# Kernel optimization log

Hardware: AMD Instinct MI355X
Metric: run time of the kernel (lower is better)

Reference implementation:

```python
import jax, jax.numpy as jnp
import numpy as np
import math

EMB = 256
H = 2
DH = EMB // H  # 128; seq_len must equal DH due to matmul(q,k) without transpose
B = 1024
S = DH


def setup_inputs() -> dict:
    key = jax.random.key(0)
    ks = jax.random.split(key, 12)
    sc = 1.0 / math.sqrt(EMB)
    return {
        "q": jax.random.normal(ks[0], (B, S, EMB), jnp.float32),
        "k": jax.random.normal(ks[1], (B, S, EMB), jnp.float32),
        "v": jax.random.normal(ks[2], (B, S, EMB), jnp.float32),
        "attention_mask": jax.random.randint(ks[3], (B, S), 0, 2, jnp.int32),
        "Wq": jax.random.normal(ks[4], (EMB, EMB), jnp.float32) * sc,
        "bq": jnp.zeros((EMB,), jnp.float32),
        "Wk": jax.random.normal(ks[5], (EMB, EMB), jnp.float32) * sc,
        "bk": jnp.zeros((EMB,), jnp.float32),
        "Wv": jax.random.normal(ks[6], (EMB, EMB), jnp.float32) * sc,
        "bv": jnp.zeros((EMB,), jnp.float32),
        "Wo": jax.random.normal(ks[7], (EMB, EMB), jnp.float32) * sc,
        "bo": jnp.zeros((EMB,), jnp.float32),
    }


def reference(q, k, v, attention_mask, Wq, bq, Wk, bk, Wv, bv, Wo, bo):
    b, s, _ = q.shape
    qp = (q @ Wq + bq) * (1.0 / math.sqrt(EMB))  # scale by sqrt(all_head_size)
    kp = k @ Wk + bk
    vp = v @ Wv + bv  # projected but unused downstream (faithful to source)
    # [B,S,E] -> [B,H,S,DH]
    qh = qp.reshape(b, s, H, DH).transpose(0, 2, 1, 3)
    kh = kp.reshape(b, s, H, DH).transpose(0, 2, 1, 3)
    # matmul WITHOUT transposing k: contract q's head dim with k's seq dim
    scores = jnp.einsum("bhsm,bhmj->bhsj", qh, kh)  # [B,H,S,DH]
    # additive mask: +1.0 where attention_mask == 0 (quirk of source)
    mask_add = (attention_mask == 0).astype(jnp.float32)[:, None, None, :]
    probs = jax.nn.softmax(scores + mask_add, axis=-1)  # [B,H,S,DH]
    out = probs.transpose(0, 2, 1, 3).reshape(b, s, H * DH)
    return out @ Wo + bo
```

## Files before the change

### kernel.cpp

```cpp
#include <hip/hip_runtime.h>
#include <hip/hip_bf16.h>

#define NB 1024
#define NS 128
#define NE 256

typedef __attribute__((ext_vector_type(8))) short bf16x8;
typedef __attribute__((ext_vector_type(4))) float f32x4;

__device__ __forceinline__ unsigned short f2bf(float x) {
  unsigned int u = __float_as_uint(x);
  u = (u + 0x7fffu + ((u >> 16) & 1u)) >> 16;
  return (unsigned short)u;
}

__global__ void prep_weights(const float* __restrict__ Wq,
                             const float* __restrict__ Wk,
                             const float* __restrict__ Wo,
                             short* __restrict__ WqT,
                             short* __restrict__ WkT,
                             short* __restrict__ WoT) {
  int idx = blockIdx.x * blockDim.x + threadIdx.x;
  int n = idx >> 8;
  int kk = idx & 255;
  WqT[idx] = (short)f2bf(Wq[kk * NE + n]);
  WkT[idx] = (short)f2bf(Wk[kk * NE + n]);
  WoT[idx] = (short)f2bf(Wo[kk * NE + n]);
}

__device__ __forceinline__ void stage_tile(const float* __restrict__ src,
                                           char* __restrict__ dst, int t) {
  #pragma unroll
  for (int i = 0; i < 16; ++i) {
    int idx = t + i * 512;
    float4 v = reinterpret_cast<const float4*>(src)[idx];
    int row = idx >> 6;
    int colb = (idx & 63) << 3;
    ushort4 u;
    u.x = f2bf(v.x); u.y = f2bf(v.y); u.z = f2bf(v.z); u.w = f2bf(v.w);
    *reinterpret_cast<ushort4*>(dst + row * 512 + (colb ^ ((row & 7) << 4))) = u;
  }
}

__device__ __forceinline__ void gemm_8x16(const char* __restrict__ ldsA,
                                          const short* __restrict__ BT,
                                          int wr, int wc, int cl, int c4,
                                          f32x4 acc[4][4]) {
  #pragma unroll
  for (int ks = 0; ks < 8; ++ks) {
    const int kel = ks * 32 + 8 * c4;
    bf16x8 a[4], bb[4];
    #pragma unroll
    for (int mi = 0; mi < 4; ++mi) {
      int row = wr * 64 + mi * 16 + cl;
      a[mi] = *reinterpret_cast<const bf16x8*>(
          ldsA + row * 512 + ((kel * 2) ^ ((row & 7) << 4)));
    }
    #pragma unroll
    for (int ni = 0; ni < 4; ++ni) {
      int col = wc * 64 + ni * 16 + cl;
      bb[ni] = *reinterpret_cast<const bf16x8*>(BT + col * 256 + kel);
    }
    #pragma unroll
    for (int mi = 0; mi < 4; ++mi)
      #pragma unroll
      for (int ni = 0; ni < 4; ++ni)
        acc[mi][ni] = __builtin_amdgcn_mfma_f32_16x16x32_bf16(
            a[mi], bb[ni], acc[mi][ni], 0, 0, 0);
  }
}

__global__ __launch_bounds__(512, 2)
void fused_attn(const float* __restrict__ q,
                const float* __restrict__ kin,
                const int* __restrict__ am,
                const float* __restrict__ bq,
                const float* __restrict__ bk,
                const float* __restrict__ bo,
                const short* __restrict__ WqT,
                const short* __restrict__ WkT,
                const short* __restrict__ WoT,
                float* __restrict__ out) {
  extern __shared__ char lds[];
  char* stA = lds;
  char* kpT = lds + 65536;

  const int t = threadIdx.x;
  const int lane = t & 63;
  const int wid = t >> 6;
  const int cl = lane & 15;
  const int c4 = lane >> 4;
  const int wr = wid >> 2;
  const int wc = wid & 3;
  const int b = blockIdx.x;

  f32x4 acc[4][4];

  stage_tile(kin + (size_t)b * (NS * NE), stA, t);
  __syncthreads();

  #pragma unroll
  for (int mi = 0; mi < 4; ++mi)
    #pragma unroll
    for (int ni = 0; ni < 4; ++ni) acc[mi][ni] = (f32x4){0.f, 0.f, 0.f, 0.f};
  gemm_8x16(stA, WkT, wr, wc, cl, c4, acc);
  #pragma unroll
  for (int mi = 0; mi < 4; ++mi)
    #pragma unroll
    for (int ni = 0; ni < 4; ++ni) {
      int ce = wc * 64 + ni * 16 + cl;
      float bkv = bk[ce];
      int h = ce >> 7, j = ce & 127;
      char* base = kpT + h * 32768 + j * 256;
      int sw = (j & 7) << 4;
      #pragma unroll
      for (int r = 0; r < 4; ++r) {
        int seq = wr * 64 + mi * 16 + c4 * 4 + r;
        *reinterpret_cast<unsigned short*>(base + ((seq * 2) ^ sw)) =
            f2bf(acc[mi][ni][r] + bkv);
      }
    }
  __syncthreads();

  stage_tile(q + (size_t)b * (NS * NE), stA, t);
  __syncthreads();

  #pragma unroll
  for (int mi = 0; mi < 4; ++mi)
    #pragma unroll
    for (int ni = 0; ni < 4; ++ni) acc[mi][ni] = (f32x4){0.f, 0.f, 0.f, 0.f};
  gemm_8x16(stA, WqT, wr, wc, cl, c4, acc);
  __syncthreads();
  #pragma unroll
  for (int mi = 0; mi < 4; ++mi)
    #pragma unroll
    for (int ni = 0; ni < 4; ++ni) {
      int ce = wc * 64 + ni * 16 + cl;
      float bqv = bq[ce];
      int ceb = ce * 2;
      #pragma unroll
      for (int r = 0; r < 4; ++r) {
        int seq = wr * 64 + mi * 16 + c4 * 4 + r;
        *reinterpret_cast<unsigned short*>(
            stA + seq * 512 + (ceb ^ ((seq & 7) << 4))) =
            f2bf((acc[mi][ni][r] + bqv) * 0.0625f);
      }
    }
  __syncthreads();

  {
    f32x4 sacc[2][8];
    #pragma unroll
    for (int h = 0; h < 2; ++h)
      #pragma unroll
      for (int ni = 0; ni < 8; ++ni) sacc[h][ni] = (f32x4){0.f, 0.f, 0.f, 0.f};
    const int arow = wid * 16 + cl;
    #pragma unroll
    for (int h = 0; h < 2; ++h) {
      #pragma unroll
      for (int ks = 0; ks < 4; ++ks) {
        int kel = h * 128 + ks * 32 + 8 * c4;
        bf16x8 a = *reinterpret_cast<const bf16x8*>(
            stA + arow * 512 + ((kel * 2) ^ ((arow & 7) << 4)));
        int kb = (ks * 32 + 8 * c4) * 2;
        #pragma unroll
        for (int ni = 0; ni < 8; ++ni) {
          int jr = ni * 16 + cl;
          bf16x8 bbv = *reinterpret_cast<const bf16x8*>(
              kpT + h * 32768 + jr * 256 + (kb ^ ((jr & 7) << 4)));
          sacc[h][ni] = __builtin_amdgcn_mfma_f32_16x16x32_bf16(
              a, bbv, sacc[h][ni], 0, 0, 0);
        }
      }
    }
    float madd[8];
    #pragma unroll
    for (int ni = 0; ni < 8; ++ni)
      madd[ni] = (am[b * NS + ni * 16 + cl] == 0) ? 1.0f : 0.0f;
    #pragma unroll
    for (int h = 0; h < 2; ++h) {
      #pragma unroll
      for (int r = 0; r < 4; ++r) {
        float m = -1e30f;
        #pragma unroll
        for (int ni = 0; ni < 8; ++ni) m = fmaxf(m, sacc[h][ni][r] + madd[ni]);
        #pragma unroll
        for (int d = 1; d < 16; d <<= 1) m = fmaxf(m, __shfl_xor(m, d, 64));
        float s = 0.f;
        #pragma unroll
        for (int ni = 0; ni < 8; ++ni) {
          float e = __expf(sacc[h][ni][r] + madd[ni] - m);
          sacc[h][ni][r] = e;
          s += e;
        }
        #pragma unroll
        for (int d = 1; d < 16; d <<= 1) s += __shfl_xor(s, d, 64);
        float rinv = 1.0f / s;
        #pragma unroll
        for (int ni = 0; ni < 8; ++ni) sacc[h][ni][r] *= rinv;
      }
    }
    #pragma unroll
    for (int h = 0; h < 2; ++h)
      #pragma unroll
      for (int ni = 0; ni < 8; ++ni)
        #pragma unroll
        for (int r = 0; r < 4; ++r) {
          int seq = wid * 16 + c4 * 4 + r;
          int ceb = (h * 128 + ni * 16 + cl) * 2;
          *reinterpret_cast<unsigned short*>(
              stA + seq * 512 + (ceb ^ ((seq & 7) << 4))) =
              f2bf(sacc[h][ni][r]);
        }
  }
  __syncthreads();

  #pragma unroll
  for (int mi = 0; mi < 4; ++mi)
    #pragma unroll
    for (int ni = 0; ni < 4; ++ni) acc[mi][ni] = (f32x4){0.f, 0.f, 0.f, 0.f};
  gemm_8x16(stA, WoT, wr, wc, cl, c4, acc);
  float* ob = out + (size_t)b * (NS * NE);
  #pragma unroll
  for (int mi = 0; mi < 4; ++mi)
    #pragma unroll
    for (int ni = 0; ni < 4; ++ni) {
      int ce = wc * 64 + ni * 16 + cl;
      float bov = bo[ce];
      #pragma unroll
      for (int r = 0; r < 4; ++r) {
        int seq = wr * 64 + mi * 16 + c4 * 4 + r;
        ob[seq * NE + ce] = acc[mi][ni][r] + bov;
      }
    }
}

extern "C" void kernel_launch(void* const* d_in, const int* in_sizes, int n_in,
                              void* d_out, int out_size, void* d_ws, size_t ws_size,
                              hipStream_t stream) {
  const float* q  = (const float*)d_in[0];
  const float* k  = (const float*)d_in[1];
  const int*   am = (const int*)d_in[3];
  const float* Wq = (const float*)d_in[4];
  const float* bq = (const float*)d_in[5];
  const float* Wk = (const float*)d_in[6];
  const float* bk = (const float*)d_in[7];
  const float* Wo = (const float*)d_in[10];
  const float* bo = (const float*)d_in[11];
  float* out = (float*)d_out;

  short* WqT = (short*)d_ws;
  short* WkT = WqT + NE * NE;
  short* WoT = WkT + NE * NE;

  prep_weights<<<NE * NE / 256, 256, 0, stream>>>(Wq, Wk, Wo, WqT, WkT, WoT);

  (void)hipFuncSetAttribute((const void*)fused_attn,
                            hipFuncAttributeMaxDynamicSharedMemorySize, 131072);
  fused_attn<<<NB, 512, 131072, stream>>>(q, k, am, bq, bk, bo,
                                          WqT, WkT, WoT, out);
}
```

Baseline: 194.1 us.

## Use 1024-thread blocks, prefetch q into registers during k staging

Doubles the block to 16 waves. Each wave now owns a 32x64 output tile, and in the scores stage each wave handles one head and one 16-row tile. Both the k and q tiles are loaded from global memory at the start, with q held in registers while the K projection runs, so the second global load latency is hidden. K-projection results are written to LDS as packed ushort4 stores. The goal is more waves to hide latency and fewer exposed load phases, at the cost of higher register pressure (launch_bounds 1024 with a min of 4) and 128KB of LDS per block, which limits residency to one block per CU.

```diff
diff --git a/kernel.cpp b/kernel.cpp
--- a/kernel.cpp
+++ b/kernel.cpp
@@ -28,31 +28,17 @@
   WoT[idx] = (short)f2bf(Wo[kk * NE + n]);
 }
 
-__device__ __forceinline__ void stage_tile(const float* __restrict__ src,
-                                           char* __restrict__ dst, int t) {
-  #pragma unroll
-  for (int i = 0; i < 16; ++i) {
-    int idx = t + i * 512;
-    float4 v = reinterpret_cast<const float4*>(src)[idx];
-    int row = idx >> 6;
-    int colb = (idx & 63) << 3;
-    ushort4 u;
-    u.x = f2bf(v.x); u.y = f2bf(v.y); u.z = f2bf(v.z); u.w = f2bf(v.w);
-    *reinterpret_cast<ushort4*>(dst + row * 512 + (colb ^ ((row & 7) << 4))) = u;
-  }
-}
-
-__device__ __forceinline__ void gemm_8x16(const char* __restrict__ ldsA,
-                                          const short* __restrict__ BT,
-                                          int wr, int wc, int cl, int c4,
-                                          f32x4 acc[4][4]) {
+__device__ __forceinline__ void gemm_2x4(const char* __restrict__ ldsA,
+                                         const short* __restrict__ BT,
+                                         int wr, int wc, int cl, int c4,
+                                         f32x4 acc[2][4]) {
   #pragma unroll
   for (int ks = 0; ks < 8; ++ks) {
     const int kel = ks * 32 + 8 * c4;
-    bf16x8 a[4], bb[4];
-    #pragma unroll
-    for (int mi = 0; mi < 4; ++mi) {
-      int row = wr * 64 + mi * 16 + cl;
+    bf16x8 a[2], bb[4];
+    #pragma unroll
+    for (int mi = 0; mi < 2; ++mi) {
+      int row = wr * 32 + mi * 16 + cl;
       a[mi] = *reinterpret_cast<const bf16x8*>(
           ldsA + row * 512 + ((kel * 2) ^ ((row & 7) << 4)));
     }
@@ -62,7 +48,7 @@
       bb[ni] = *reinterpret_cast<const bf16x8*>(BT + col * 256 + kel);
     }
     #pragma unroll
-    for (int mi = 0; mi < 4; ++mi)
+    for (int mi = 0; mi < 2; ++mi)
       #pragma unroll
       for (int ni = 0; ni < 4; ++ni)
         acc[mi][ni] = __builtin_amdgcn_mfma_f32_16x16x32_bf16(
@@ -70,7 +56,7 @@
   }
 }
 
-__global__ __launch_bounds__(512, 2)
+__global__ __launch_bounds__(1024, 4)
 void fused_attn(const float* __restrict__ q,
                 const float* __restrict__ kin,
                 const int* __restrict__ am,
@@ -82,8 +68,8 @@
                 const short* __restrict__ WoT,
                 float* __restrict__ out) {
   extern __shared__ char lds[];
-  char* stA = lds;
-  char* kpT = lds + 65536;
+  char* ST = lds;
+  char* KT = lds + 65536;
 
   const int t = threadIdx.x;
   const int lane = t & 63;
@@ -94,45 +80,72 @@
   const int wc = wid & 3;
   const int b = blockIdx.x;
 
-  f32x4 acc[4][4];
-
-  stage_tile(kin + (size_t)b * (NS * NE), stA, t);
-  __syncthreads();
-
-  #pragma unroll
-  for (int mi = 0; mi < 4; ++mi)
+  const float* qb = q + (size_t)b * (NS * NE);
+  const float* kb = kin + (size_t)b * (NS * NE);
+
+  f32x4 acc[2][4];
+
+  float4 qv[8];
+  {
+    const float4* k4 = reinterpret_cast<const float4*>(kb);
+    const float4* q4 = reinterpret_cast<const float4*>(qb);
+    #pragma unroll
+    for (int i = 0; i < 8; ++i) {
+      int idx = t + i * 1024;
+      float4 v = k4[idx];
+      qv[i] = q4[idx];
+      int row = idx >> 6;
+      int colb = (idx & 63) << 3;
+      ushort4 u;
+      u.x = f2bf(v.x); u.y = f2bf(v.y); u.z = f2bf(v.z); u.w = f2bf(v.w);
+      *reinterpret_cast<ushort4*>(ST + row * 512 + (colb ^ ((row & 7) << 4))) = u;
+    }
+  }
+  __syncthreads();
+
+  #pragma unroll
+  for (int mi = 0; mi < 2; ++mi)
     #pragma unroll
     for (int ni = 0; ni < 4; ++ni) acc[mi][ni] = (f32x4){0.f, 0.f, 0.f, 0.f};
-  gemm_8x16(stA, WkT, wr, wc, cl, c4, acc);
-  #pragma unroll
-  for (int mi = 0; mi < 4; ++mi)
+  gemm_2x4(ST, WkT, wr, wc, cl, c4, acc);
+  #pragma unroll
+  for (int mi = 0; mi < 2; ++mi)
     #pragma unroll
     for (int ni = 0; ni < 4; ++ni) {
       int ce = wc * 64 + ni * 16 + cl;
       float bkv = bk[ce];
       int h = ce >> 7, j = ce & 127;
-      char* base = kpT + h * 32768 + j * 256;
-      int sw = (j & 7) << 4;
-      #pragma unroll
-      for (int r = 0; r < 4; ++r) {
-        int seq = wr * 64 + mi * 16 + c4 * 4 + r;
-        *reinterpret_cast<unsigned short*>(base + ((seq * 2) ^ sw)) =
-            f2bf(acc[mi][ni][r] + bkv);
-      }
-    }
-  __syncthreads();
-
-  stage_tile(q + (size_t)b * (NS * NE), stA, t);
-  __syncthreads();
-
-  #pragma unroll
-  for (int mi = 0; mi < 4; ++mi)
+      int seq0 = wr * 32 + mi * 16 + c4 * 4;
+      ushort4 u;
+      u.x = f2bf(acc[mi][ni][0] + bkv);
+      u.y = f2bf(acc[mi][ni][1] + bkv);
+      u.z = f2bf(acc[mi][ni][2] + bkv);
+      u.w = f2bf(acc[mi][ni][3] + bkv);
+      *reinterpret_cast<ushort4*>(
+          KT + h * 32768 + j * 256 + ((seq0 * 2) ^ ((j & 7) << 4))) = u;
+    }
+  __syncthreads();
+
+  #pragma unroll
+  for (int i = 0; i < 8; ++i) {
+    int idx = t + i * 1024;
+    int row = idx >> 6;
+    int colb = (idx & 63) << 3;
+    ushort4 u;
+    u.x = f2bf(qv[i].x); u.y = f2bf(qv[i].y);
+    u.z = f2bf(qv[i].z); u.w = f2bf(qv[i].w);
+    *reinterpret_cast<ushort4*>(ST + row * 512 + (colb ^ ((row & 7) << 4))) = u;
+  }
+  __syncthreads();
+
+  #pragma unroll
+  for (int mi = 0; mi < 2; ++mi)
     #pragma unroll
     for (int ni = 0; ni < 4; ++ni) acc[mi][ni] = (f32x4){0.f, 0.f, 0.f, 0.f};
-  gemm_8x16(stA, WqT, wr, wc, cl, c4, acc);
-  __syncthreads();
-  #pragma unroll
-  for (int mi = 0; mi < 4; ++mi)
+  gemm_2x4(ST, WqT, wr, wc, cl, c4, acc);
+  __syncthreads();
+  #pragma unroll
+  for (int mi = 0; mi < 2; ++mi)
     #pragma unroll
     for (int ni = 0; ni < 4; ++ni) {
       int ce = wc * 64 + ni * 16 + cl;
@@ -140,37 +153,34 @@
       int ceb = ce * 2;
       #pragma unroll
       for (int r = 0; r < 4; ++r) {
-        int seq = wr * 64 + mi * 16 + c4 * 4 + r;
+        int seq = wr * 32 + mi * 16 + c4 * 4 + r;
         *reinterpret_cast<unsigned short*>(
-            stA + seq * 512 + (ceb ^ ((seq & 7) << 4))) =
+            ST + seq * 512 + (ceb ^ ((seq & 7) << 4))) =
             f2bf((acc[mi][ni][r] + bqv) * 0.0625f);
       }
     }
   __syncthreads();
 
   {
-    f32x4 sacc[2][8];
-    #pragma unroll
-    for (int h = 0; h < 2; ++h)
-      #pragma unroll
-      for (int ni = 0; ni < 8; ++ni) sacc[h][ni] = (f32x4){0.f, 0.f, 0.f, 0.f};
-    const int arow = wid * 16 + cl;
-    #pragma unroll
-    for (int h = 0; h < 2; ++h) {
-      #pragma unroll
-      for (int ks = 0; ks < 4; ++ks) {
-        int kel = h * 128 + ks * 32 + 8 * c4;
-        bf16x8 a = *reinterpret_cast<const bf16x8*>(
-            stA + arow * 512 + ((kel * 2) ^ ((arow & 7) << 4)));
-        int kb = (ks * 32 + 8 * c4) * 2;
-        #pragma unroll
-        for (int ni = 0; ni < 8; ++ni) {
-          int jr = ni * 16 + cl;
-          bf16x8 bbv = *reinterpret_cast<const bf16x8*>(
-              kpT + h * 32768 + jr * 256 + (kb ^ ((jr & 7) << 4)));
-          sacc[h][ni] = __builtin_amdgcn_mfma_f32_16x16x32_bf16(
-              a, bbv, sacc[h][ni], 0, 0, 0);
-        }
+    const int h = wid >> 3;
+    const int rt = wid & 7;
+    f32x4 sacc[8];
+    #pragma unroll
+    for (int ni = 0; ni < 8; ++ni) sacc[ni] = (f32x4){0.f, 0.f, 0.f, 0.f};
+    const int arow = rt * 16 + cl;
+    #pragma unroll
+    for (int ks = 0; ks < 4; ++ks) {
+      int kel = h * 128 + ks * 32 + 8 * c4;
+      bf16x8 a = *reinterpret_cast<const bf16x8*>(
+          ST + arow * 512 + ((kel * 2) ^ ((arow & 7) << 4)));
+      int kb2 = (ks * 32 + 8 * c4) * 2;
+      #pragma unroll
+      for (int ni = 0; ni < 8; ++ni) {
+        int jr = ni * 16 + cl;
+        bf16x8 bbv = *reinterpret_cast<const bf16x8*>(
+            KT + h * 32768 + jr * 256 + (kb2 ^ ((jr & 7) << 4)));
+        sacc[ni] = __builtin_amdgcn_mfma_f32_16x16x32_bf16(
+            a, bbv, sacc[ni], 0, 0, 0);
       }
     }
     float madd[8];
@@ -178,58 +188,52 @@
     for (int ni = 0; ni < 8; ++ni)
       madd[ni] = (am[b * NS + ni * 16 + cl] == 0) ? 1.0f : 0.0f;
     #pragma unroll
-    for (int h = 0; h < 2; ++h) {
+    for (int r = 0; r < 4; ++r) {
+      float m = -1e30f;
+      #pragma unroll
+      for (int ni = 0; ni < 8; ++ni) m = fmaxf(m, sacc[ni][r] + madd[ni]);
+      #pragma unroll
+      for (int d = 1; d < 16; d <<= 1) m = fmaxf(m, __shfl_xor(m, d, 64));
+      float s = 0.f;
+      #pragma unroll
+      for (int ni = 0; ni < 8; ++ni) {
+        float e = __expf(sacc[ni][r] + madd[ni] - m);
+        sacc[ni][r] = e;
+        s += e;
+      }
+      #pragma unroll
+      for (int d = 1; d < 16; d <<= 1) s += __shfl_xor(s, d, 64);
+      float rinv = 1.0f / s;
+      #pragma unroll
+      for (int ni = 0; ni < 8; ++ni) sacc[ni][r] *= rinv;
+    }
+    #pragma unroll
+    for (int ni = 0; ni < 8; ++ni)
       #pragma unroll
       for (int r = 0; r < 4; ++r) {
-        float m = -1e30f;
-        #pragma unroll
-        for (int ni = 0; ni < 8; ++ni) m = fmaxf(m, sacc[h][ni][r] + madd[ni]);
-        #pragma unroll
-        for (int d = 1; d < 16; d <<= 1) m = fmaxf(m, __shfl_xor(m, d, 64));
-        float s = 0.f;
-        #pragma unroll
-        for (int ni = 0; ni < 8; ++ni) {
-          float e = __expf(sacc[h][ni][r] + madd[ni] - m);
-          sacc[h][ni][r] = e;
-          s += e;
-        }
-        #pragma unroll
-        for (int d = 1; d < 16; d <<= 1) s += __shfl_xor(s, d, 64);
-        float rinv = 1.0f / s;
-        #pragma unroll
-        for (int ni = 0; ni < 8; ++ni) sacc[h][ni][r] *= rinv;
-      }
-    }
-    #pragma unroll
-    for (int h = 0; h < 2; ++h)
-      #pragma unroll
-      for (int ni = 0; ni < 8; ++ni)
-        #pragma unroll
-        for (int r = 0; r < 4; ++r) {
-          int seq = wid * 16 + c4 * 4 + r;
-          int ceb = (h * 128 + ni * 16 + cl) * 2;
-          *reinterpret_cast<unsigned short*>(
-              stA + seq * 512 + (ceb ^ ((seq & 7) << 4))) =
-              f2bf(sacc[h][ni][r]);
-        }
-  }
-  __syncthreads();
-
-  #pragma unroll
-  for (int mi = 0; mi < 4; ++mi)
+        int row = rt * 16 + c4 * 4 + r;
+        int ceb = (h * 128 + ni * 16 + cl) * 2;
+        *reinterpret_cast<unsigned short*>(
+            ST + row * 512 + (ceb ^ ((row & 7) << 4))) = f2bf(sacc[ni][r]);
+      }
+  }
+  __syncthreads();
+
+  #pragma unroll
+  for (int mi = 0; mi < 2; ++mi)
     #pragma unroll
     for (int ni = 0; ni < 4; ++ni) acc[mi][ni] = (f32x4){0.f, 0.f, 0.f, 0.f};
-  gemm_8x16(stA, WoT, wr, wc, cl, c4, acc);
+  gemm_2x4(ST, WoT, wr, wc, cl, c4, acc);
   float* ob = out + (size_t)b * (NS * NE);
   #pragma unroll
-  for (int mi = 0; mi < 4; ++mi)
+  for (int mi = 0; mi < 2; ++mi)
     #pragma unroll
     for (int ni = 0; ni < 4; ++ni) {
       int ce = wc * 64 + ni * 16 + cl;
       float bov = bo[ce];
       #pragma unroll
       for (int r = 0; r < 4; ++r) {
-        int seq = wr * 64 + mi * 16 + c4 * 4 + r;
+        int seq = wr * 32 + mi * 16 + c4 * 4 + r;
         ob[seq * NE + ce] = acc[mi][ni][r] + bov;
       }
     }
@@ -257,6 +261,6 @@
 
   (void)hipFuncSetAttribute((const void*)fused_attn,
                             hipFuncAttributeMaxDynamicSharedMemorySize, 131072);
-  fused_attn<<<NB, 512, 131072, stream>>>(q, k, am, bq, bk, bo,
-                                          WqT, WkT, WoT, out);
-}
+  fused_attn<<<NB, 1024, 131072, stream>>>(q, k, am, bq, bk, bo,
+                                           WqT, WkT, WoT, out);
+}
```

New measurement: 275.3 us. 1.42x slower.

## Split fused attention into parallel QK projection and attention-output kernels

Applied to the files above, without the earlier changes.

Splits the single fused kernel into two. The first launches two blocks per batch, one projecting K (stored transposed) and one projecting Q, writing bf16 results to workspace. The second reloads them, runs scores, softmax and the output projection. Each kernel now uses 64KB of LDS instead of 128KB, allowing more resident blocks and twice as many blocks in the projection stage. The cost is an extra global round-trip of roughly 128MB of bf16 intermediates. The old fused kernel is kept as a fallback when the workspace is too small.

```diff
diff --git a/kernel.cpp b/kernel.cpp
--- a/kernel.cpp
+++ b/kernel.cpp
@@ -68,6 +68,208 @@
         acc[mi][ni] = __builtin_amdgcn_mfma_f32_16x16x32_bf16(
             a[mi], bb[ni], acc[mi][ni], 0, 0, 0);
   }
+}
+
+__global__ __launch_bounds__(512, 4)
+void proj_qk(const float* __restrict__ q,
+             const float* __restrict__ kin,
+             const float* __restrict__ bq,
+             const float* __restrict__ bk,
+             const short* __restrict__ WqT,
+             const short* __restrict__ WkT,
+             short* __restrict__ QP,
+             short* __restrict__ KPT) {
+  extern __shared__ char ST[];
+  const int t = threadIdx.x;
+  const int lane = t & 63;
+  const int wid = t >> 6;
+  const int cl = lane & 15;
+  const int c4 = lane >> 4;
+  const int b = blockIdx.x >> 1;
+
+  if ((blockIdx.x & 1) == 0) {
+    stage_tile(kin + (size_t)b * (NS * NE), ST, t);
+    __syncthreads();
+    const int we = wid >> 1;
+    const int wm = wid & 1;
+    f32x4 acc[4][4];
+    #pragma unroll
+    for (int ei = 0; ei < 4; ++ei)
+      #pragma unroll
+      for (int mi = 0; mi < 4; ++mi) acc[ei][mi] = (f32x4){0.f, 0.f, 0.f, 0.f};
+    #pragma unroll
+    for (int ks = 0; ks < 8; ++ks) {
+      const int kel = ks * 32 + 8 * c4;
+      bf16x8 a[4], bb[4];
+      #pragma unroll
+      for (int ei = 0; ei < 4; ++ei) {
+        int er = we * 64 + ei * 16 + cl;
+        a[ei] = *reinterpret_cast<const bf16x8*>(WkT + er * 256 + kel);
+      }
+      #pragma unroll
+      for (int mi = 0; mi < 4; ++mi) {
+        int mr = wm * 64 + mi * 16 + cl;
+        bb[mi] = *reinterpret_cast<const bf16x8*>(
+            ST + mr * 512 + ((kel * 2) ^ ((mr & 7) << 4)));
+      }
+      #pragma unroll
+      for (int ei = 0; ei < 4; ++ei)
+        #pragma unroll
+        for (int mi = 0; mi < 4; ++mi)
+          acc[ei][mi] = __builtin_amdgcn_mfma_f32_16x16x32_bf16(
+              a[ei], bb[mi], acc[ei][mi], 0, 0, 0);
+    }
+    short* kp = KPT + (size_t)b * (NE * NS);
+    #pragma unroll
+    for (int ei = 0; ei < 4; ++ei)
+      #pragma unroll
+      for (int r = 0; r < 4; ++r) {
+        int e = we * 64 + ei * 16 + c4 * 4 + r;
+        float bkv = bk[e];
+        #pragma unroll
+        for (int mi = 0; mi < 4; ++mi) {
+          int m = wm * 64 + mi * 16 + cl;
+          kp[e * NS + m] = (short)f2bf(acc[ei][mi][r] + bkv);
+        }
+      }
+  } else {
+    stage_tile(q + (size_t)b * (NS * NE), ST, t);
+    __syncthreads();
+    const int wr = wid >> 2, wc = wid & 3;
+    f32x4 acc[4][4];
+    #pragma unroll
+    for (int mi = 0; mi < 4; ++mi)
+      #pragma unroll
+      for (int ni = 0; ni < 4; ++ni) acc[mi][ni] = (f32x4){0.f, 0.f, 0.f, 0.f};
+    gemm_8x16(ST, WqT, wr, wc, cl, c4, acc);
+    char* qp = (char*)QP + (size_t)b * 65536;
+    #pragma unroll
+    for (int mi = 0; mi < 4; ++mi)
+      #pragma unroll
+      for (int ni = 0; ni < 4; ++ni) {
+        int ce = wc * 64 + ni * 16 + cl;
+        float bqv = bq[ce];
+        #pragma unroll
+        for (int r = 0; r < 4; ++r) {
+          int seq = wr * 64 + mi * 16 + c4 * 4 + r;
+          *reinterpret_cast<unsigned short*>(
+              qp + seq * 512 + ((ce * 2) ^ ((seq & 7) << 4))) =
+              f2bf((acc[mi][ni][r] + bqv) * 0.0625f);
+        }
+      }
+  }
+}
+
+__global__ __launch_bounds__(512, 4)
+void attn_out(const short* __restrict__ QP,
+              const short* __restrict__ KPT,
+              const int* __restrict__ am,
+              const float* __restrict__ bo,
+              const short* __restrict__ WoT,
+              float* __restrict__ out) {
+  extern __shared__ char ST[];
+  const int t = threadIdx.x;
+  const int lane = t & 63;
+  const int wid = t >> 6;
+  const int cl = lane & 15;
+  const int c4 = lane >> 4;
+  const int b = blockIdx.x;
+
+  {
+    const int4* src = reinterpret_cast<const int4*>((const char*)QP + (size_t)b * 65536);
+    int4* dst = reinterpret_cast<int4*>(ST);
+    #pragma unroll
+    for (int i = 0; i < 8; ++i) dst[t + i * 512] = src[t + i * 512];
+  }
+  __syncthreads();
+
+  {
+    const short* kp = KPT + (size_t)b * (NE * NS);
+    f32x4 sacc[2][8];
+    #pragma unroll
+    for (int h = 0; h < 2; ++h)
+      #pragma unroll
+      for (int ni = 0; ni < 8; ++ni) sacc[h][ni] = (f32x4){0.f, 0.f, 0.f, 0.f};
+    const int arow = wid * 16 + cl;
+    #pragma unroll
+    for (int h = 0; h < 2; ++h) {
+      #pragma unroll
+      for (int ks = 0; ks < 4; ++ks) {
+        int kel = h * 128 + ks * 32 + 8 * c4;
+        bf16x8 a = *reinterpret_cast<const bf16x8*>(
+            ST + arow * 512 + ((kel * 2) ^ ((arow & 7) << 4)));
+        int mel = ks * 32 + 8 * c4;
+        #pragma unroll
+        for (int ni = 0; ni < 8; ++ni) {
+          int jr = ni * 16 + cl;
+          bf16x8 bbv = *reinterpret_cast<const bf16x8*>(
+              kp + (h * 128 + jr) * NS + mel);
+          sacc[h][ni] = __builtin_amdgcn_mfma_f32_16x16x32_bf16(
+              a, bbv, sacc[h][ni], 0, 0, 0);
+        }
+      }
+    }
+    float madd[8];
+    #pragma unroll
+    for (int ni = 0; ni < 8; ++ni)
+      madd[ni] = (am[b * NS + ni * 16 + cl] == 0) ? 1.0f : 0.0f;
+    #pragma unroll
+    for (int h = 0; h < 2; ++h) {
+      #pragma unroll
+      for (int r = 0; r < 4; ++r) {
+        float m = -1e30f;
+        #pragma unroll
+        for (int ni = 0; ni < 8; ++ni) m = fmaxf(m, sacc[h][ni][r] + madd[ni]);
+        #pragma unroll
+        for (int d = 1; d < 16; d <<= 1) m = fmaxf(m, __shfl_xor(m, d, 64));
+        float s = 0.f;
+        #pragma unroll
+        for (int ni = 0; ni < 8; ++ni) {
+          float e = __expf(sacc[h][ni][r] + madd[ni] - m);
+          sacc[h][ni][r] = e;
+          s += e;
+        }
+        #pragma unroll
+        for (int d = 1; d < 16; d <<= 1) s += __shfl_xor(s, d, 64);
+        float rinv = 1.0f / s;
+        #pragma unroll
+        for (int ni = 0; ni < 8; ++ni) sacc[h][ni][r] *= rinv;
+      }
+    }
+    #pragma unroll
+    for (int h = 0; h < 2; ++h)
+      #pragma unroll
+      for (int ni = 0; ni < 8; ++ni)
+        #pragma unroll
+        for (int r = 0; r < 4; ++r) {
+          int row = wid * 16 + c4 * 4 + r;
+          int ceb = (h * 128 + ni * 16 + cl) * 2;
+          *reinterpret_cast<unsigned short*>(
+              ST + row * 512 + (ceb ^ ((row & 7) << 4))) = f2bf(sacc[h][ni][r]);
+        }
+  }
+  __syncthreads();
+
+  const int wr = wid >> 2, wc = wid & 3;
+  f32x4 acc[4][4];
+  #pragma unroll
+  for (int mi = 0; mi < 4; ++mi)
+    #pragma unroll
+    for (int ni = 0; ni < 4; ++ni) acc[mi][ni] = (f32x4){0.f, 0.f, 0.f, 0.f};
+  gemm_8x16(ST, WoT, wr, wc, cl, c4, acc);
+  float* ob = out + (size_t)b * (NS * NE);
+  #pragma unroll
+  for (int mi = 0; mi < 4; ++mi)
+    #pragma unroll
+    for (int ni = 0; ni < 4; ++ni) {
+      int ce = wc * 64 + ni * 16 + cl;
+      float bov = bo[ce];
+      #pragma unroll
+      for (int r = 0; r < 4; ++r) {
+        int seq = wr * 64 + mi * 16 + c4 * 4 + r;
+        ob[seq * NE + ce] = acc[mi][ni][r] + bov;
+      }
+    }
 }
 
 __global__ __launch_bounds__(512, 2)
@@ -84,7 +286,6 @@
   extern __shared__ char lds[];
   char* stA = lds;
   char* kpT = lds + 65536;
-
   const int t = threadIdx.x;
   const int lane = t & 63;
   const int wid = t >> 6;
@@ -93,12 +294,10 @@
   const int wr = wid >> 2;
   const int wc = wid & 3;
   const int b = blockIdx.x;
-
   f32x4 acc[4][4];
 
   stage_tile(kin + (size_t)b * (NS * NE), stA, t);
   __syncthreads();
-
   #pragma unroll
   for (int mi = 0; mi < 4; ++mi)
     #pragma unroll
@@ -121,10 +320,8 @@
       }
     }
   __syncthreads();
-
   stage_tile(q + (size_t)b * (NS * NE), stA, t);
   __syncthreads();
-
   #pragma unroll
   for (int mi = 0; mi < 4; ++mi)
     #pragma unroll
@@ -147,7 +344,6 @@
       }
     }
   __syncthreads();
-
   {
     f32x4 sacc[2][8];
     #pragma unroll
@@ -209,12 +405,10 @@
           int seq = wid * 16 + c4 * 4 + r;
           int ceb = (h * 128 + ni * 16 + cl) * 2;
           *reinterpret_cast<unsigned short*>(
-              stA + seq * 512 + (ceb ^ ((seq & 7) << 4))) =
-              f2bf(sacc[h][ni][r]);
-        }
-  }
-  __syncthreads();
-
+              stA + seq * 512 + (ceb ^ ((seq & 7) << 4))) = f2bf(sacc[h][ni][r]);
+        }
+  }
+  __syncthreads();
   #pragma unroll
   for (int mi = 0; mi < 4; ++mi)
     #pragma unroll
@@ -252,11 +446,19 @@
   short* WqT = (short*)d_ws;
   short* WkT = WqT + NE * NE;
   short* WoT = WkT + NE * NE;
+  short* QP  = WoT + NE * NE;
+  short* KPT = QP + (size_t)NB * NS * NE;
 
   prep_weights<<<NE * NE / 256, 256, 0, stream>>>(Wq, Wk, Wo, WqT, WkT, WoT);
 
-  (void)hipFuncSetAttribute((const void*)fused_attn,
-                            hipFuncAttributeMaxDynamicSharedMemorySize, 131072);
-  fused_attn<<<NB, 512, 131072, stream>>>(q, k, am, bq, bk, bo,
-                                          WqT, WkT, WoT, out);
-}
+  const size_t need = 3ULL * NE * NE * 2 + 2ULL * NB * NS * NE * 2;
+  if (ws_size >= need) {
+    proj_qk<<<2 * NB, 512, 65536, stream>>>(q, k, bq, bk, WqT, WkT, QP, KPT);
+    attn_out<<<NB, 512, 65536, stream>>>(QP, KPT, am, bo, WoT, out);
+  } else {
+    (void)hipFuncSetAttribute((const void*)fused_attn,
+                              hipFuncAttributeMaxDynamicSharedMemorySize, 131072);
+    fused_attn<<<NB, 512, 131072, stream>>>(q, k, am, bq, bk, bo,
+                                            WqT, WkT, WoT, out);
+  }
+}
```

Result: slower. 257.7 us (+32.8%).

## Restructure fused attention to compute transposed projections straight from global memory, halving LDS

Applied to the files above, without the earlier changes.

Projections are now computed in transposed form (weights as A, inputs as B), loading fp32 inputs straight from global memory and converting them in registers instead of staging them through LDS. Q projections stay packed in registers and feed the score MFMA with zero-padded operands. The 1/16 scale is folded into Wq, and LDS use drops from 128KB to 64KB to target higher occupancy (launch bounds 4). The trade-off is redundant global reads of the input tiles across waves and wasted MFMA work on the zero-padded half of each score operand.

```diff
diff --git a/kernel.cpp b/kernel.cpp
--- a/kernel.cpp
+++ b/kernel.cpp
@@ -8,10 +8,29 @@
 typedef __attribute__((ext_vector_type(8))) short bf16x8;
 typedef __attribute__((ext_vector_type(4))) float f32x4;
 
+union BF8 { bf16x8 v; unsigned u[4]; unsigned short s[8]; };
+
 __device__ __forceinline__ unsigned short f2bf(float x) {
-  unsigned int u = __float_as_uint(x);
+  unsigned u = __float_as_uint(x);
   u = (u + 0x7fffu + ((u >> 16) & 1u)) >> 16;
   return (unsigned short)u;
+}
+
+__device__ __forceinline__ unsigned packbf(float lo, float hi) {
+  return (unsigned)f2bf(lo) | ((unsigned)f2bf(hi) << 16);
+}
+
+__device__ __forceinline__ bf16x8 cvt8(float4 lo, float4 hi) {
+  BF8 r;
+  r.u[0] = packbf(lo.x, lo.y);
+  r.u[1] = packbf(lo.z, lo.w);
+  r.u[2] = packbf(hi.x, hi.y);
+  r.u[3] = packbf(hi.z, hi.w);
+  return r.v;
+}
+
+__device__ __forceinline__ f32x4 MF(bf16x8 a, bf16x8 b, f32x4 c) {
+  return __builtin_amdgcn_mfma_f32_16x16x32_bf16(a, b, c, 0, 0, 0);
 }
 
 __global__ void prep_weights(const float* __restrict__ Wq,
@@ -23,216 +42,243 @@
   int idx = blockIdx.x * blockDim.x + threadIdx.x;
   int n = idx >> 8;
   int kk = idx & 255;
-  WqT[idx] = (short)f2bf(Wq[kk * NE + n]);
+  WqT[idx] = (short)f2bf(Wq[kk * NE + n] * 0.0625f);
   WkT[idx] = (short)f2bf(Wk[kk * NE + n]);
   WoT[idx] = (short)f2bf(Wo[kk * NE + n]);
 }
 
-__device__ __forceinline__ void stage_tile(const float* __restrict__ src,
-                                           char* __restrict__ dst, int t) {
-  #pragma unroll
-  for (int i = 0; i < 16; ++i) {
-    int idx = t + i * 512;
-    float4 v = reinterpret_cast<const float4*>(src)[idx];
-    int row = idx >> 6;
-    int colb = (idx & 63) << 3;
-    ushort4 u;
-    u.x = f2bf(v.x); u.y = f2bf(v.y); u.z = f2bf(v.z); u.w = f2bf(v.w);
-    *reinterpret_cast<ushort4*>(dst + row * 512 + (colb ^ ((row & 7) << 4))) = u;
-  }
-}
-
-__device__ __forceinline__ void gemm_8x16(const char* __restrict__ ldsA,
-                                          const short* __restrict__ BT,
-                                          int wr, int wc, int cl, int c4,
-                                          f32x4 acc[4][4]) {
+__device__ __forceinline__ void gemm_halfT(const short* __restrict__ WT,
+                                           const float* __restrict__ inp,
+                                           int h, int sb, int cl, int c4,
+                                           f32x4 acc[8][2]) {
   #pragma unroll
   for (int ks = 0; ks < 8; ++ks) {
-    const int kel = ks * 32 + 8 * c4;
-    bf16x8 a[4], bb[4];
-    #pragma unroll
-    for (int mi = 0; mi < 4; ++mi) {
-      int row = wr * 64 + mi * 16 + cl;
-      a[mi] = *reinterpret_cast<const bf16x8*>(
-          ldsA + row * 512 + ((kel * 2) ^ ((row & 7) << 4)));
-    }
-    #pragma unroll
-    for (int ni = 0; ni < 4; ++ni) {
-      int col = wc * 64 + ni * 16 + cl;
-      bb[ni] = *reinterpret_cast<const bf16x8*>(BT + col * 256 + kel);
-    }
-    #pragma unroll
-    for (int mi = 0; mi < 4; ++mi)
-      #pragma unroll
-      for (int ni = 0; ni < 4; ++ni)
-        acc[mi][ni] = __builtin_amdgcn_mfma_f32_16x16x32_bf16(
-            a[mi], bb[ni], acc[mi][ni], 0, 0, 0);
-  }
-}
-
-__global__ __launch_bounds__(512, 2)
-void fused_attn(const float* __restrict__ q,
-                const float* __restrict__ kin,
-                const int* __restrict__ am,
-                const float* __restrict__ bq,
-                const float* __restrict__ bk,
-                const float* __restrict__ bo,
-                const short* __restrict__ WqT,
-                const short* __restrict__ WkT,
-                const short* __restrict__ WoT,
-                float* __restrict__ out) {
-  extern __shared__ char lds[];
-  char* stA = lds;
-  char* kpT = lds + 65536;
-
+    bf16x8 bb[2];
+    #pragma unroll
+    for (int ct = 0; ct < 2; ++ct) {
+      const float* rp = inp + (sb * 32 + ct * 16 + cl) * NE + ks * 32 + c4 * 8;
+      bb[ct] = cvt8(*reinterpret_cast<const float4*>(rp),
+                    *reinterpret_cast<const float4*>(rp + 4));
+    }
+    #pragma unroll
+    for (int eh = 0; eh < 2; ++eh) {
+      bf16x8 a[4];
+      #pragma unroll
+      for (int e4 = 0; e4 < 4; ++e4) {
+        int et = eh * 4 + e4;
+        a[e4] = *reinterpret_cast<const bf16x8*>(
+            WT + (h * 128 + et * 16 + cl) * NE + ks * 32 + c4 * 8);
+      }
+      #pragma unroll
+      for (int e4 = 0; e4 < 4; ++e4)
+        #pragma unroll
+        for (int ct = 0; ct < 2; ++ct)
+          acc[eh * 4 + e4][ct] = MF(a[e4], bb[ct], acc[eh * 4 + e4][ct]);
+    }
+  }
+}
+
+__global__ __launch_bounds__(512, 4)
+void fused_attn2(const float* __restrict__ q,
+                 const float* __restrict__ kin,
+                 const int* __restrict__ am,
+                 const short* __restrict__ WqT,
+                 const short* __restrict__ WkT,
+                 const short* __restrict__ WoT,
+                 const float* __restrict__ bq,
+                 const float* __restrict__ bk,
+                 const float* __restrict__ bo,
+                 float* __restrict__ out) {
+  __shared__ char LB[65536];
   const int t = threadIdx.x;
   const int lane = t & 63;
   const int wid = t >> 6;
   const int cl = lane & 15;
   const int c4 = lane >> 4;
-  const int wr = wid >> 2;
-  const int wc = wid & 3;
+  const int h = wid >> 2;
+  const int sb = wid & 3;
   const int b = blockIdx.x;
-
-  f32x4 acc[4][4];
-
-  stage_tile(kin + (size_t)b * (NS * NE), stA, t);
+  const float* qb = q + (size_t)b * (NS * NE);
+  const float* kb = kin + (size_t)b * (NS * NE);
+
+  {
+    f32x4 acc[8][2];
+    #pragma unroll
+    for (int et = 0; et < 8; ++et)
+      #pragma unroll
+      for (int ct = 0; ct < 2; ++ct) acc[et][ct] = (f32x4){0.f, 0.f, 0.f, 0.f};
+    gemm_halfT(WkT, kb, h, sb, cl, c4, acc);
+    #pragma unroll
+    for (int et = 0; et < 8; ++et) {
+      int e0 = h * 128 + et * 16 + c4 * 4;
+      float4 bk4 = *reinterpret_cast<const float4*>(bk + e0);
+      #pragma unroll
+      for (int mt = 0; mt < 2; ++mt) {
+        int m = sb * 32 + mt * 16 + cl;
+        #pragma unroll
+        for (int r = 0; r < 4; ++r) {
+          int e = e0 + r;
+          float bv = (r == 0) ? bk4.x : (r == 1) ? bk4.y : (r == 2) ? bk4.z : bk4.w;
+          *reinterpret_cast<unsigned short*>(
+              LB + e * 256 + ((m * 2) ^ ((e & 7) << 4))) =
+              f2bf(acc[et][mt][r] + bv);
+        }
+      }
+    }
+  }
+
+  unsigned qpk[8][2][2];
+  {
+    f32x4 acc[8][2];
+    #pragma unroll
+    for (int et = 0; et < 8; ++et)
+      #pragma unroll
+      for (int ct = 0; ct < 2; ++ct) acc[et][ct] = (f32x4){0.f, 0.f, 0.f, 0.f};
+    gemm_halfT(WqT, qb, h, sb, cl, c4, acc);
+    #pragma unroll
+    for (int et = 0; et < 8; ++et) {
+      int e0 = h * 128 + et * 16 + c4 * 4;
+      float4 bq4 = *reinterpret_cast<const float4*>(bq + e0);
+      #pragma unroll
+      for (int st = 0; st < 2; ++st) {
+        qpk[et][st][0] = packbf(acc[et][st][0] + bq4.x * 0.0625f,
+                                acc[et][st][1] + bq4.y * 0.0625f);
+        qpk[et][st][1] = packbf(acc[et][st][2] + bq4.z * 0.0625f,
+                                acc[et][st][3] + bq4.w * 0.0625f);
+      }
+    }
+  }
   __syncthreads();
 
-  #pragma unroll
-  for (int mi = 0; mi < 4; ++mi)
-    #pragma unroll
-    for (int ni = 0; ni < 4; ++ni) acc[mi][ni] = (f32x4){0.f, 0.f, 0.f, 0.f};
-  gemm_8x16(stA, WkT, wr, wc, cl, c4, acc);
-  #pragma unroll
-  for (int mi = 0; mi < 4; ++mi)
-    #pragma unroll
-    for (int ni = 0; ni < 4; ++ni) {
-      int ce = wc * 64 + ni * 16 + cl;
-      float bkv = bk[ce];
-      int h = ce >> 7, j = ce & 127;
-      char* base = kpT + h * 32768 + j * 256;
-      int sw = (j & 7) << 4;
+  f32x4 sacc[8][2];
+  #pragma unroll
+  for (int jt = 0; jt < 8; ++jt)
+    #pragma unroll
+    for (int st = 0; st < 2; ++st) sacc[jt][st] = (f32x4){0.f, 0.f, 0.f, 0.f};
+  #pragma unroll
+  for (int ks = 0; ks < 8; ++ks) {
+    BF8 bb[2];
+    #pragma unroll
+    for (int st = 0; st < 2; ++st) {
+      bb[st].u[0] = qpk[ks][st][0]; bb[st].u[1] = qpk[ks][st][1];
+      bb[st].u[2] = 0; bb[st].u[3] = 0;
+    }
+    #pragma unroll
+    for (int jh = 0; jh < 2; ++jh) {
+      BF8 a[4];
+      #pragma unroll
+      for (int j4 = 0; j4 < 4; ++j4) {
+        int jt = jh * 4 + j4;
+        uint2 d = *reinterpret_cast<const uint2*>(
+            LB + (h * 128 + jt * 16 + cl) * 256 +
+            ((ks * 32 + c4 * 8) ^ ((cl & 7) << 4)));
+        a[j4].u[0] = d.x; a[j4].u[1] = d.y; a[j4].u[2] = 0; a[j4].u[3] = 0;
+      }
+      #pragma unroll
+      for (int j4 = 0; j4 < 4; ++j4)
+        #pragma unroll
+        for (int st = 0; st < 2; ++st)
+          sacc[jh * 4 + j4][st] = MF(a[j4].v, bb[st].v, sacc[jh * 4 + j4][st]);
+    }
+  }
+
+  #pragma unroll
+  for (int jt = 0; jt < 8; ++jt) {
+    int4 mv = *reinterpret_cast<const int4*>(am + b * NS + jt * 16 + c4 * 4);
+    float m0 = (mv.x == 0) ? 1.f : 0.f;
+    float m1 = (mv.y == 0) ? 1.f : 0.f;
+    float m2 = (mv.z == 0) ? 1.f : 0.f;
+    float m3 = (mv.w == 0) ? 1.f : 0.f;
+    #pragma unroll
+    for (int st = 0; st < 2; ++st) {
+      sacc[jt][st][0] += m0;
+      sacc[jt][st][1] += m1;
+      sacc[jt][st][2] += m2;
+      sacc[jt][st][3] += m3;
+    }
+  }
+
+  float rinv[2];
+  #pragma unroll
+  for (int st = 0; st < 2; ++st) {
+    float mx = -1e30f;
+    #pragma unroll
+    for (int jt = 0; jt < 8; ++jt)
+      #pragma unroll
+      for (int r = 0; r < 4; ++r) mx = fmaxf(mx, sacc[jt][st][r]);
+    mx = fmaxf(mx, __shfl_xor(mx, 16, 64));
+    mx = fmaxf(mx, __shfl_xor(mx, 32, 64));
+    float sum = 0.f;
+    #pragma unroll
+    for (int jt = 0; jt < 8; ++jt)
       #pragma unroll
       for (int r = 0; r < 4; ++r) {
-        int seq = wr * 64 + mi * 16 + c4 * 4 + r;
-        *reinterpret_cast<unsigned short*>(base + ((seq * 2) ^ sw)) =
-            f2bf(acc[mi][ni][r] + bkv);
-      }
-    }
+        float ev = __expf(sacc[jt][st][r] - mx);
+        sacc[jt][st][r] = ev;
+        sum += ev;
+      }
+    sum += __shfl_xor(sum, 16, 64);
+    sum += __shfl_xor(sum, 32, 64);
+    rinv[st] = 1.0f / sum;
+  }
   __syncthreads();
 
-  stage_tile(q + (size_t)b * (NS * NE), stA, t);
+  #pragma unroll
+  for (int st = 0; st < 2; ++st) {
+    int s = sb * 32 + st * 16 + cl;
+    #pragma unroll
+    for (int jt = 0; jt < 8; ++jt) {
+      uint2 w;
+      w.x = packbf(sacc[jt][st][0] * rinv[st], sacc[jt][st][1] * rinv[st]);
+      w.y = packbf(sacc[jt][st][2] * rinv[st], sacc[jt][st][3] * rinv[st]);
+      *reinterpret_cast<uint2*>(
+          LB + s * 512 + ((h * 256 + jt * 32 + c4 * 8) ^ ((s & 7) << 4))) = w;
+    }
+  }
   __syncthreads();
 
-  #pragma unroll
-  for (int mi = 0; mi < 4; ++mi)
-    #pragma unroll
-    for (int ni = 0; ni < 4; ++ni) acc[mi][ni] = (f32x4){0.f, 0.f, 0.f, 0.f};
-  gemm_8x16(stA, WqT, wr, wc, cl, c4, acc);
-  __syncthreads();
-  #pragma unroll
-  for (int mi = 0; mi < 4; ++mi)
-    #pragma unroll
-    for (int ni = 0; ni < 4; ++ni) {
-      int ce = wc * 64 + ni * 16 + cl;
-      float bqv = bq[ce];
-      int ceb = ce * 2;
-      #pragma unroll
-      for (int r = 0; r < 4; ++r) {
-        int seq = wr * 64 + mi * 16 + c4 * 4 + r;
-        *reinterpret_cast<unsigned short*>(
-            stA + seq * 512 + (ceb ^ ((seq & 7) << 4))) =
-            f2bf((acc[mi][ni][r] + bqv) * 0.0625f);
-      }
-    }
-  __syncthreads();
-
   {
-    f32x4 sacc[2][8];
-    #pragma unroll
-    for (int h = 0; h < 2; ++h)
-      #pragma unroll
-      for (int ni = 0; ni < 8; ++ni) sacc[h][ni] = (f32x4){0.f, 0.f, 0.f, 0.f};
-    const int arow = wid * 16 + cl;
-    #pragma unroll
-    for (int h = 0; h < 2; ++h) {
-      #pragma unroll
-      for (int ks = 0; ks < 4; ++ks) {
-        int kel = h * 128 + ks * 32 + 8 * c4;
-        bf16x8 a = *reinterpret_cast<const bf16x8*>(
-            stA + arow * 512 + ((kel * 2) ^ ((arow & 7) << 4)));
-        int kb = (ks * 32 + 8 * c4) * 2;
-        #pragma unroll
-        for (int ni = 0; ni < 8; ++ni) {
-          int jr = ni * 16 + cl;
-          bf16x8 bbv = *reinterpret_cast<const bf16x8*>(
-              kpT + h * 32768 + jr * 256 + (kb ^ ((jr & 7) << 4)));
-          sacc[h][ni] = __builtin_amdgcn_mfma_f32_16x16x32_bf16(
-              a, bbv, sacc[h][ni], 0, 0, 0);
+    const int wr = h, wc = sb;
+    f32x4 acc[4][4];
+    #pragma unroll
+    for (int mi = 0; mi < 4; ++mi)
+      #pragma unroll
+      for (int ni = 0; ni < 4; ++ni) acc[mi][ni] = (f32x4){0.f, 0.f, 0.f, 0.f};
+    #pragma unroll
+    for (int ks = 0; ks < 8; ++ks) {
+      const int kel = ks * 32 + c4 * 8;
+      bf16x8 a[4], bb[4];
+      #pragma unroll
+      for (int mi = 0; mi < 4; ++mi) {
+        int row = wr * 64 + mi * 16 + cl;
+        a[mi] = *reinterpret_cast<const bf16x8*>(
+            LB + row * 512 + ((kel * 2) ^ ((row & 7) << 4)));
+      }
+      #pragma unroll
+      for (int ni = 0; ni < 4; ++ni) {
+        int col = wc * 64 + ni * 16 + cl;
+        bb[ni] = *reinterpret_cast<const bf16x8*>(WoT + col * NE + kel);
+      }
+      #pragma unroll
+      for (int mi = 0; mi < 4; ++mi)
+        #pragma unroll
+        for (int ni = 0; ni < 4; ++ni)
+          acc[mi][ni] = MF(a[mi], bb[ni], acc[mi][ni]);
+    }
+    float* ob = out + (size_t)b * (NS * NE);
+    #pragma unroll
+    for (int mi = 0; mi < 4; ++mi)
+      #pragma unroll
+      for (int ni = 0; ni < 4; ++ni) {
+        int ce = wc * 64 + ni * 16 + cl;
+        float bov = bo[ce];
+        #pragma unroll
+        for (int r = 0; r < 4; ++r) {
+          int seq = wr * 64 + mi * 16 + c4 * 4 + r;
+          ob[seq * NE + ce] = acc[mi][ni][r] + bov;
         }
       }
-    }
-    float madd[8];
-    #pragma unroll
-    for (int ni = 0; ni < 8; ++ni)
-      madd[ni] = (am[b * NS + ni * 16 + cl] == 0) ? 1.0f : 0.0f;
-    #pragma unroll
-    for (int h = 0; h < 2; ++h) {
-      #pragma unroll
-      for (int r = 0; r < 4; ++r) {
-        float m = -1e30f;
-        #pragma unroll
-        for (int ni = 0; ni < 8; ++ni) m = fmaxf(m, sacc[h][ni][r] + madd[ni]);
-        #pragma unroll
-        for (int d = 1; d < 16; d <<= 1) m = fmaxf(m, __shfl_xor(m, d, 64));
-        float s = 0.f;
-        #pragma unroll
-        for (int ni = 0; ni < 8; ++ni) {
-          float e = __expf(sacc[h][ni][r] + madd[ni] - m);
-          sacc[h][ni][r] = e;
-          s += e;
-        }
-        #pragma unroll
-        for (int d = 1; d < 16; d <<= 1) s += __shfl_xor(s, d, 64);
-        float rinv = 1.0f / s;
-        #pragma unroll
-        for (int ni = 0; ni < 8; ++ni) sacc[h][ni][r] *= rinv;
-      }
-    }
-    #pragma unroll
-    for (int h = 0; h < 2; ++h)
-      #pragma unroll
-      for (int ni = 0; ni < 8; ++ni)
-        #pragma unroll
-        for (int r = 0; r < 4; ++r) {
-          int seq = wid * 16 + c4 * 4 + r;
-          int ceb = (h * 128 + ni * 16 + cl) * 2;
-          *reinterpret_cast<unsigned short*>(
-              stA + seq * 512 + (ceb ^ ((seq & 7) << 4))) =
-              f2bf(sacc[h][ni][r]);
-        }
-  }
-  __syncthreads();
-
-  #pragma unroll
-  for (int mi = 0; mi < 4; ++mi)
-    #pragma unroll
-    for (int ni = 0; ni < 4; ++ni) acc[mi][ni] = (f32x4){0.f, 0.f, 0.f, 0.f};
-  gemm_8x16(stA, WoT, wr, wc, cl, c4, acc);
-  float* ob = out + (size_t)b * (NS * NE);
-  #pragma unroll
-  for (int mi = 0; mi < 4; ++mi)
-    #pragma unroll
-    for (int ni = 0; ni < 4; ++ni) {
-      int ce = wc * 64 + ni * 16 + cl;
-      float bov = bo[ce];
-      #pragma unroll
-      for (int r = 0; r < 4; ++r) {
-        int seq = wr * 64 + mi * 16 + c4 * 4 + r;
-        ob[seq * NE + ce] = acc[mi][ni][r] + bov;
-      }
-    }
+  }
 }
 
 extern "C" void kernel_launch(void* const* d_in, const int* in_sizes, int n_in,
@@ -254,9 +300,5 @@
   short* WoT = WkT + NE * NE;
 
   prep_weights<<<NE * NE / 256, 256, 0, stream>>>(Wq, Wk, Wo, WqT, WkT, WoT);
-
-  (void)hipFuncSetAttribute((const void*)fused_attn,
-                            hipFuncAttributeMaxDynamicSharedMemorySize, 131072);
-  fused_attn<<<NB, 512, 131072, stream>>>(q, k, am, bq, bk, bo,
-                                          WqT, WkT, WoT, out);
-}
+  fused_attn2<<<NB, 512, 0, stream>>>(q, k, am, WqT, WkT, WoT, bq, bk, bo, out);
+}
```

Result: slower. 280.4 us (+44.5%).
